# Kernel optimization log

Measured on AMD Instinct MI355X. Metric: run time of the kernel, lower is better.

Reference implementation:

```python
import jax, jax.numpy as jnp
import numpy as np

B, T, S, H = 8, 256, 256, 512


def setup_inputs() -> dict:
    key = jax.random.key(0)
    k1, k2, k3, k4, k5, k6, k7 = jax.random.split(key, 7)
    query = jax.random.normal(k1, (B, T, H), dtype=jnp.float32)
    encoder_outputs = jax.random.normal(k2, (B, S, H), dtype=jnp.float32)
    src_lengths = jax.random.randint(k3, (B,), 1, S + 1)
    src_lengths = src_lengths.at[0].set(S)  # ensure max(lengths) == S (torch code masks to lengths.max())
    scale = 1.0 / np.sqrt(H)
    W_s = jax.random.normal(k4, (H, H), dtype=jnp.float32) * scale      # nn.Linear(H,H) weight
    W_h = jax.random.normal(k5, (H, H), dtype=jnp.float32) * scale
    v = jax.random.normal(k6, (H,), dtype=jnp.float32) * scale          # nn.Linear(H,1) weight
    W_out = jax.random.normal(k7, (H, 2 * H), dtype=jnp.float32) * scale  # nn.Linear(2H,H) weight
    return {"query": query, "encoder_outputs": encoder_outputs, "src_lengths": src_lengths,
            "W_s": W_s, "W_h": W_h, "v": v, "W_out": W_out}


def reference(query, encoder_outputs, src_lengths, W_s, W_h, v, W_out):
    # torch Linear: y = x @ W.T
    Ws_q = jnp.einsum('bth,oh->bto', query, W_s)            # (B,T,H)
    Wh_e = jnp.einsum('bsh,oh->bso', encoder_outputs, W_h)  # (B,S,H)
    # score(i,j) = v^T tanh(Ws_q_j + Wh_e_i), broadcast over (B,T,S,H)
    energies = jnp.einsum('btsh,h->bts',
                          jnp.tanh(Ws_q[:, :, None, :] + Wh_e[:, None, :, :]), v)
    mask = jnp.arange(encoder_outputs.shape[1]) < src_lengths[:, None]  # (B,S)
    energies = jnp.where(mask[:, None, :], energies, -jnp.inf)
    attn_weights = jax.nn.softmax(energies, axis=-1)        # (B,T,S)
    context = jnp.einsum('bts,bsh->bth', attn_weights, encoder_outputs)
    combined = jnp.concatenate([context, query], axis=-1)   # (B,T,2H)
    attn_out = jnp.tanh(jnp.einsum('btk,ok->bto', combined, W_out))
    return attn_out
```

## Files before the change

kernel.cpp:

```cpp
#include <hip/hip_runtime.h>
#include <hip/hip_bf16.h>


typedef __attribute__((ext_vector_type(8))) short bf16x8;
typedef __attribute__((ext_vector_type(4))) float floatx4;

#define C2LOG2E 2.8853900817779268f
#define LOG2E   1.4426950408889634f
#define NEGBIG  -1e30f

__device__ __forceinline__ float fexp2(float x) { return __builtin_amdgcn_exp2f(x); }
__device__ __forceinline__ float frcp(float x)  { return __builtin_amdgcn_rcpf(x); }
__device__ __forceinline__ float ftanh(float x) {
    return 1.0f - 2.0f * frcp(1.0f + fexp2(C2LOG2E * x));
}
__device__ __forceinline__ float fexp2x(float x) {
    return fexp2(C2LOG2E * x);
}

__device__ __forceinline__ unsigned int f2bf_bits(float f) {
    unsigned int u = __float_as_uint(f);
    return (u + 0x7fffu + ((u >> 16) & 1u)) >> 16;
}

typedef const __attribute__((address_space(1))) unsigned int* gas_u32p;
typedef __attribute__((address_space(3))) unsigned int* las_u32p;
__device__ __forceinline__ void gload16(const void* g, void* l) {
    __builtin_amdgcn_global_load_lds((gas_u32p)g, (las_u32p)l, 16, 0, 0);
}

__global__ __launch_bounds__(256) void cast_all_bf16(
    const float* __restrict__ q,  const float* __restrict__ e,
    const float* __restrict__ Ws, const float* __restrict__ Wh,
    const float* __restrict__ Wo,
    unsigned short* __restrict__ qb,  unsigned short* __restrict__ eb,
    unsigned short* __restrict__ Wsb, unsigned short* __restrict__ Whb,
    unsigned short* __restrict__ Wob)
{
    int blk = blockIdx.x;
    const float* src; unsigned short* dst; int base;
    if      (blk < 1024) { src = q;  dst = qb;  base = blk; }
    else if (blk < 2048) { src = e;  dst = eb;  base = blk - 1024; }
    else if (blk < 2304) { src = Ws; dst = Wsb; base = blk - 2048; }
    else if (blk < 2560) { src = Wh; dst = Whb; base = blk - 2304; }
    else                 { src = Wo; dst = Wob; base = blk - 2560; }
    size_t i = (size_t)base * 1024 + threadIdx.x * 4;
    float4 f = *(const float4*)(src + i);
    ushort4 o;
    o.x = (unsigned short)f2bf_bits(f.x);
    o.y = (unsigned short)f2bf_bits(f.y);
    o.z = (unsigned short)f2bf_bits(f.z);
    o.w = (unsigned short)f2bf_bits(f.w);
    *(ushort4*)(dst + i) = o;
}

__global__ __launch_bounds__(256) void gemm32x64_exp_dual(
    const unsigned short* __restrict__ Xa, const unsigned short* __restrict__ Wa,
    float* __restrict__ Ca,
    const unsigned short* __restrict__ Xb, const unsigned short* __restrict__ Wb_,
    float* __restrict__ Cb)
{
    __shared__ unsigned short sA[32 * 64];
    __shared__ unsigned short sB[64 * 64];
    const int K = 512;
    int blk = blockIdx.x;
    const unsigned short* X; const unsigned short* W; float* C;
    int mt, nt, N;
    if (blk < 512) { X = Xa; W = Wa; C = Ca; N = 512;  mt = blk >> 3; nt = blk & 7; }
    else { blk -= 512; X = Xb; W = Wb_; C = Cb; N = 2048; mt = blk >> 5; nt = blk & 31; }
    int row0 = mt * 32, col0 = nt * 64;
    int tid = threadIdx.x, lane = tid & 63, w = tid >> 6;
    int mw = (w & 1) * 16, nw = (w >> 1) * 32;
    int r = lane & 15;

    int lr  = lane >> 3;
    int csw = ((lane & 7) ^ lr) << 3;
    const unsigned short* gA  = X + (size_t)(row0 + 8 * w + lr) * K + csw;
    const unsigned short* gB0 = W + (size_t)(col0 + 16 * w + lr) * K + csw;
    const unsigned short* gB1 = W + (size_t)(col0 + 16 * w + 8 + lr) * K + csw;
    unsigned short* lA  = &sA[w * 512];
    unsigned short* lB0 = &sB[w * 1024];
    unsigned short* lB1 = &sB[w * 1024 + 512];

    int xr = (r & 7) << 4;
    int cq = (lane >> 4) << 4;
    const char* cA = (const char*)sA;
    const char* cB = (const char*)sB;
    int a0 = (mw + r) * 128 + (cq ^ xr);
    int a1 = (mw + r) * 128 + ((cq + 64) ^ xr);
    int b0 = (nw + r) * 128 + (cq ^ xr);
    int b1 = (nw + r) * 128 + ((cq + 64) ^ xr);

    floatx4 acc0 = {0,0,0,0}, acc1 = {0,0,0,0};
    gload16(gA, lA); gload16(gB0, lB0); gload16(gB1, lB1);

    for (int kb = 0; kb < 8; ++kb) {
        __syncthreads();
        bf16x8 af0 = *(const bf16x8*)(cA + a0);
        bf16x8 af1 = *(const bf16x8*)(cA + a1);
        bf16x8 b00 = *(const bf16x8*)(cB + b0);
        bf16x8 b10 = *(const bf16x8*)(cB + b0 + 2048);
        bf16x8 b01 = *(const bf16x8*)(cB + b1);
        bf16x8 b11 = *(const bf16x8*)(cB + b1 + 2048);
        acc0 = __builtin_amdgcn_mfma_f32_16x16x32_bf16(af0, b00, acc0, 0, 0, 0);
        acc1 = __builtin_amdgcn_mfma_f32_16x16x32_bf16(af0, b10, acc1, 0, 0, 0);
        acc0 = __builtin_amdgcn_mfma_f32_16x16x32_bf16(af1, b01, acc0, 0, 0, 0);
        acc1 = __builtin_amdgcn_mfma_f32_16x16x32_bf16(af1, b11, acc1, 0, 0, 0);
        if (kb < 7) {
            __syncthreads();
            gA += 64; gB0 += 64; gB1 += 64;
            gload16(gA, lA); gload16(gB0, lB0); gload16(gB1, lB1);
        }
    }
    int rq = (lane >> 4) * 4;
    float* cp = C + (size_t)(row0 + mw + rq) * N + col0 + nw + r;
#pragma unroll
    for (int i = 0; i < 4; ++i) {
        cp[(size_t)i * N]      = fexp2x(acc0[i]);
        cp[(size_t)i * N + 16] = fexp2x(acc1[i]);
    }
}

#define TQ 4
__global__ __launch_bounds__(512) void energies_v6(
    const float* __restrict__ EA,
    const float* __restrict__ EBT,
    const float* __restrict__ Vv,
    const int* __restrict__ Len,
    float* __restrict__ E)
{
    __shared__ float sA[TQ][516];
    __shared__ float sWn[512];
    __shared__ float sRed[8][TQ][130];

    int tid  = threadIdx.x;
    int lane = tid & 63;
    int w    = tid >> 6;
    int blk  = blockIdx.x;
    int b    = blk >> 7;
    int j    = (blk >> 6) & 1;
    int tq   = blk & 63;
    int len  = Len[b];
    if (j * 128 >= len) return;
    int row0g = b * 256 + tq * TQ;

    {
        int t = tid >> 7, c = (tid & 127) * 4;
        *(float4*)&sA[t][c] = *(const float4*)(EA + (size_t)(row0g + t) * 512 + c);
        sWn[tid] = -2.0f * Vv[tid];
    }
    __syncthreads();

    int h0 = w * 64;
    float acc[TQ][2] = {{0.f}};
    const float* bt = EBT + (size_t)h0 * 2048 + b * 256 + j * 128 + lane;

    float B[8], P[8];
#pragma unroll
    for (int i = 0; i < 4; ++i) {
        B[i]     = bt[(size_t)i * 2048];
        B[i + 4] = bt[(size_t)i * 2048 + 64];
    }
#pragma unroll
    for (int hh = 0; hh < 64; hh += 4) {
        if (hh + 4 < 64) {
            const float* nb = bt + (size_t)(hh + 4) * 2048;
#pragma unroll
            for (int i = 0; i < 4; ++i) {
                P[i]     = nb[(size_t)i * 2048];
                P[i + 4] = nb[(size_t)i * 2048 + 64];
            }
        }
        float4 w4 = *(const float4*)&sWn[h0 + hh];
#pragma unroll
        for (int t = 0; t < TQ; ++t) {
            float4 a4 = *(const float4*)&sA[t][h0 + hh];
#pragma unroll
            for (int u = 0; u < 2; ++u) {
                float d0 = fmaf(a4.x, B[4 * u + 0], 1.0f);
                float d1 = fmaf(a4.y, B[4 * u + 1], 1.0f);
                float d2 = fmaf(a4.z, B[4 * u + 2], 1.0f);
                float d3 = fmaf(a4.w, B[4 * u + 3], 1.0f);
                float num01 = fmaf(w4.x, d1, w4.y * d0);
                float num23 = fmaf(w4.z, d3, w4.w * d2);
                acc[t][u] = fmaf(num01, frcp(d0 * d1), acc[t][u]);
                acc[t][u] = fmaf(num23, frcp(d2 * d3), acc[t][u]);
            }
        }
#pragma unroll
        for (int i = 0; i < 8; ++i) B[i] = P[i];
    }

#pragma unroll
    for (int t = 0; t < TQ; ++t) {
        sRed[w][t][lane]      = acc[t][0];
        sRed[w][t][lane + 64] = acc[t][1];
    }
    __syncthreads();
    {
        int t = tid >> 7, s = tid & 127;
        float sum = 0.f;
#pragma unroll
        for (int ww = 0; ww < 8; ++ww) sum += sRed[ww][t][s];
        E[(size_t)(row0g + t) * 256 + j * 128 + s] = sum;
    }
}

__global__ __launch_bounds__(512) void softmax_ctx_fused(
    const float* __restrict__ E,
    const unsigned short* __restrict__ Eb,
    const int* __restrict__ Len,
    unsigned short* __restrict__ Ctx)
{
    __shared__ unsigned short EncT[64][264];
    __shared__ unsigned short sWb[64][264];
    int tid = threadIdx.x, lane = tid & 63, w = tid >> 6;
    int blk = blockIdx.x;
    int b = blk & 7, hq = (blk >> 3) & 7, tg = blk >> 6;
    int len = Len[b];

    {
        int s = tid >> 1, hg = (tid & 1) * 32;
        const ushort4* src = (const ushort4*)(Eb + (size_t)(b * 256 + s) * 512 + hq * 64 + hg);
#pragma unroll
        for (int k = 0; k < 8; ++k) {
            ushort4 u = src[k];
            EncT[hg + k * 4 + 0][s] = u.x;
            EncT[hg + k * 4 + 1][s] = u.y;
            EncT[hg + k * 4 + 2][s] = u.z;
            EncT[hg + k * 4 + 3][s] = u.w;
        }
    }
    for (int i = 0; i < 8; ++i) {
        int row = w * 8 + i;
        const float* erow = E + (size_t)(b * 256 + tg * 64 + row) * 256;
        float ev[4];
#pragma unroll
        for (int j = 0; j < 4; ++j) {
            int s = lane + 64 * j;
            ev[j] = (s < len) ? erow[s] : NEGBIG;
        }
        float m = fmaxf(fmaxf(ev[0], ev[1]), fmaxf(ev[2], ev[3]));
#pragma unroll
        for (int o = 1; o < 64; o <<= 1) m = fmaxf(m, __shfl_xor(m, o, 64));
        float wv[4], wsum = 0.f;
#pragma unroll
        for (int j = 0; j < 4; ++j) { wv[j] = fexp2((ev[j] - m) * LOG2E); wsum += wv[j]; }
#pragma unroll
        for (int o = 1; o < 64; o <<= 1) wsum += __shfl_xor(wsum, o, 64);
        float inv = frcp(wsum);
#pragma unroll
        for (int j = 0; j < 4; ++j)
            sWb[row][lane + 64 * j] = (unsigned short)f2bf_bits(wv[j] * inv);
    }
    __syncthreads();

    int mt = w & 3, npair = w >> 2;
    int t0 = mt * 16;
    int r  = lane & 15, kq = (lane >> 4) * 8;
    int n0 = npair * 32 + r;
    floatx4 acc0 = {0.f,0.f,0.f,0.f}, acc1 = {0.f,0.f,0.f,0.f};
#pragma unroll
    for (int k = 0; k < 8; ++k) {
        bf16x8 a  = *(const bf16x8*)(&sWb[t0 + r][kq + 32 * k]);
        bf16x8 b0 = *(const bf16x8*)(&EncT[n0][kq + 32 * k]);
        bf16x8 b1 = *(const bf16x8*)(&EncT[n0 + 16][kq + 32 * k]);
        acc0 = __builtin_amdgcn_mfma_f32_16x16x32_bf16(a, b0, acc0, 0, 0, 0);
        acc1 = __builtin_amdgcn_mfma_f32_16x16x32_bf16(a, b1, acc1, 0, 0, 0);
    }
    int row0 = (lane >> 4) * 4;
    unsigned short* op = Ctx + (size_t)(b * 256 + tg * 64 + t0 + row0) * 512 + hq * 64 + npair * 32 + r;
#pragma unroll
    for (int i = 0; i < 4; ++i) {
        op[i * 512]      = (unsigned short)f2bf_bits(acc0[i]);
        op[i * 512 + 16] = (unsigned short)f2bf_bits(acc1[i]);
    }
}

__global__ __launch_bounds__(256) void out_gemm32x64_tanh(
    const unsigned short* __restrict__ Ctx, const unsigned short* __restrict__ Q,
    const unsigned short* __restrict__ Wout, float* __restrict__ Out)
{
    __shared__ unsigned short sA[32 * 64];
    __shared__ unsigned short sB[64 * 64];
    const int N = 512, KW = 1024;
    int blk = blockIdx.x;
    int mt = blk >> 3, nt = blk & 7;
    int row0 = mt * 32, col0 = nt * 64;
    int tid = threadIdx.x, lane = tid & 63, w = tid >> 6;
    int mw = (w & 1) * 16, nw = (w >> 1) * 32;
    int r = lane & 15;

    int lr  = lane >> 3;
    int csw = ((lane & 7) ^ lr) << 3;
    const unsigned short* gactx = Ctx  + (size_t)(row0 + 8 * w + lr) * 512 + csw;
    const unsigned short* gaq   = Q    + (size_t)(row0 + 8 * w + lr) * 512 + csw;
    const unsigned short* gB0   = Wout + (size_t)(col0 + 16 * w + lr) * KW + csw;
    const unsigned short* gB1   = Wout + (size_t)(col0 + 16 * w + 8 + lr) * KW + csw;
    unsigned short* lA  = &sA[w * 512];
    unsigned short* lB0 = &sB[w * 1024];
    unsigned short* lB1 = &sB[w * 1024 + 512];

    int xr = (r & 7) << 4;
    int cq = (lane >> 4) << 4;
    const char* cA = (const char*)sA;
    const char* cB = (const char*)sB;
    int a0 = (mw + r) * 128 + (cq ^ xr);
    int a1 = (mw + r) * 128 + ((cq + 64) ^ xr);
    int b0 = (nw + r) * 128 + (cq ^ xr);
    int b1 = (nw + r) * 128 + ((cq + 64) ^ xr);

    floatx4 acc0 = {0,0,0,0}, acc1 = {0,0,0,0};
    gload16(gactx, lA); gload16(gB0, lB0); gload16(gB1, lB1);

    for (int kb = 0; kb < 16; ++kb) {
        __syncthreads();
        bf16x8 af0 = *(const bf16x8*)(cA + a0);
        bf16x8 af1 = *(const bf16x8*)(cA + a1);
        bf16x8 b00 = *(const bf16x8*)(cB + b0);
        bf16x8 b10 = *(const bf16x8*)(cB + b0 + 2048);
        bf16x8 b01 = *(const bf16x8*)(cB + b1);
        bf16x8 b11 = *(const bf16x8*)(cB + b1 + 2048);
        acc0 = __builtin_amdgcn_mfma_f32_16x16x32_bf16(af0, b00, acc0, 0, 0, 0);
        acc1 = __builtin_amdgcn_mfma_f32_16x16x32_bf16(af0, b10, acc1, 0, 0, 0);
        acc0 = __builtin_amdgcn_mfma_f32_16x16x32_bf16(af1, b01, acc0, 0, 0, 0);
        acc1 = __builtin_amdgcn_mfma_f32_16x16x32_bf16(af1, b11, acc1, 0, 0, 0);
        if (kb < 15) {
            __syncthreads();
            int kn = kb + 1;
            const unsigned short* ga = (kn < 8 ? gactx : gaq) + (kn & 7) * 64;
            gB0 += 64; gB1 += 64;
            gload16(ga, lA); gload16(gB0, lB0); gload16(gB1, lB1);
        }
    }
    int rq = (lane >> 4) * 4;
    float* op = Out + (size_t)(row0 + mw + rq) * N + col0 + nw + r;
#pragma unroll
    for (int i = 0; i < 4; ++i) {
        op[(size_t)i * N]      = ftanh(acc0[i]);
        op[(size_t)i * N + 16] = ftanh(acc1[i]);
    }
}

extern "C" void kernel_launch(void* const* d_in, const int* in_sizes, int n_in,
                              void* d_out, int out_size, void* d_ws, size_t ws_size,
                              hipStream_t stream)
{
    const float* query = (const float*)d_in[0];
    const float* enc   = (const float*)d_in[1];
    const int*   len   = (const int*)d_in[2];
    const float* Ws    = (const float*)d_in[3];
    const float* Wh    = (const float*)d_in[4];
    const float* v     = (const float*)d_in[5];
    const float* Wout  = (const float*)d_in[6];
    float* out = (float*)d_out;

    float* EA   = (float*)d_ws;
    float* EBT  = EA + 2048 * 512;
    float* E    = EBT + 512 * 2048;
    unsigned short* qb  = (unsigned short*)(E + 2048 * 256);
    unsigned short* eb  = qb + 2048 * 512;
    unsigned short* Wsb = eb + 2048 * 512;
    unsigned short* Whb = Wsb + 512 * 512;
    unsigned short* Wob = Whb + 512 * 512;
    unsigned short* ctx = Wob + 512 * 1024;

    cast_all_bf16<<<3072, 256, 0, stream>>>(query, enc, Ws, Wh, Wout,
                                            qb, eb, Wsb, Whb, Wob);
    gemm32x64_exp_dual<<<1024, 256, 0, stream>>>(qb, Wsb, EA, Whb, eb, EBT);
    energies_v6<<<1024, 512, 0, stream>>>(EA, EBT, v, len, E);
    softmax_ctx_fused<<<256, 512, 0, stream>>>(E, eb, len, ctx);
    out_gemm32x64_tanh<<<512, 256, 0, stream>>>(ctx, qb, Wob, out);
}
```

Before: 123.2 us.

## Fuse all five stages into one cooperative persistent kernel with grid syncs

Replaces the five separate kernel launches (cast, dual GEMM, energies, softmax+context, output GEMM) with a single cooperative persistent kernel. Each stage loops over virtual blocks and the stages are separated by grid.sync(). The goal is to remove launch overhead and the gaps between kernels. In exchange it fixes the grid size by occupancy (capped at 512 blocks), uses 66KB of shared memory per block, and pays for four grid-wide barriers. The multi-launch path is kept as a fallback if the cooperative launch fails.

```diff
diff --git a/kernel.cpp b/kernel.cpp
--- a/kernel.cpp
+++ b/kernel.cpp
@@ -1,5 +1,8 @@
 #include <hip/hip_runtime.h>
 #include <hip/hip_bf16.h>
+#include <hip/hip_cooperative_groups.h>
+
+namespace cg = cooperative_groups;
 
 
 typedef __attribute__((ext_vector_type(8))) short bf16x8;
@@ -8,6 +11,7 @@
 #define C2LOG2E 2.8853900817779268f
 #define LOG2E   1.4426950408889634f
 #define NEGBIG  -1e30f
+#define TQ 4
 
 __device__ __forceinline__ float fexp2(float x) { return __builtin_amdgcn_exp2f(x); }
 __device__ __forceinline__ float frcp(float x)  { return __builtin_amdgcn_rcpf(x); }
@@ -27,6 +31,315 @@
 typedef __attribute__((address_space(3))) unsigned int* las_u32p;
 __device__ __forceinline__ void gload16(const void* g, void* l) {
     __builtin_amdgcn_global_load_lds((gas_u32p)g, (las_u32p)l, 16, 0, 0);
+}
+
+__device__ __forceinline__ void cast_range(const float* __restrict__ s,
+                                           unsigned short* __restrict__ d,
+                                           int n4, int gtid, int gs)
+{
+    for (int i = gtid; i < n4; i += gs) {
+        float4 f = ((const float4*)s)[i];
+        ushort4 o;
+        o.x = (unsigned short)f2bf_bits(f.x);
+        o.y = (unsigned short)f2bf_bits(f.y);
+        o.z = (unsigned short)f2bf_bits(f.z);
+        o.w = (unsigned short)f2bf_bits(f.w);
+        ((ushort4*)d)[i] = o;
+    }
+}
+
+__global__ __launch_bounds__(512, 4) void bahdanau_mega(
+    const float* __restrict__ q, const float* __restrict__ e,
+    const int* __restrict__ Len, const float* __restrict__ Ws,
+    const float* __restrict__ Wh, const float* __restrict__ Vv,
+    const float* __restrict__ Wout, float* __restrict__ Out,
+    float* __restrict__ EA, float* __restrict__ EBT, float* __restrict__ E,
+    unsigned short* __restrict__ qb, unsigned short* __restrict__ eb,
+    unsigned short* __restrict__ Wsb, unsigned short* __restrict__ Whb,
+    unsigned short* __restrict__ Wob, unsigned short* __restrict__ ctx)
+{
+    cg::grid_group grid = cg::this_grid();
+    __shared__ __align__(16) char smem[67584];
+
+    const int rb = blockIdx.x, G = gridDim.x;
+    const int tid = threadIdx.x, lane = tid & 63, w = tid >> 6;
+
+    {
+        int gtid = rb * 512 + tid, gs = G * 512;
+        cast_range(q,   qb,  262144, gtid, gs);
+        cast_range(e,   eb,  262144, gtid, gs);
+        cast_range(Ws,  Wsb,  65536, gtid, gs);
+        cast_range(Wh,  Whb,  65536, gtid, gs);
+        cast_range(Wout,Wob, 131072, gtid, gs);
+    }
+    grid.sync();
+
+    {
+        int g = w >> 2, wl = w & 3;
+        unsigned short* sAg = (unsigned short*)(smem + g * 12288);
+        unsigned short* sBg = (unsigned short*)(smem + g * 12288 + 4096);
+        for (int vb = rb * 2 + g; vb < 1024; vb += G * 2) {
+            __syncthreads();
+            int blk = vb;
+            const unsigned short *X, *W; float* C; int mt, nt, N;
+            if (blk < 512) { X = qb; W = Wsb; C = EA; N = 512;  mt = blk >> 3; nt = blk & 7; }
+            else { blk -= 512; X = Whb; W = eb; C = EBT; N = 2048; mt = blk >> 5; nt = blk & 31; }
+            int row0 = mt * 32, col0 = nt * 64;
+            int mw = (wl & 1) * 16, nw = (wl >> 1) * 32;
+            int r = lane & 15;
+            int lr  = lane >> 3;
+            int csw = ((lane & 7) ^ lr) << 3;
+            const unsigned short* gA  = X + (size_t)(row0 + 8 * wl + lr) * 512 + csw;
+            const unsigned short* gB0 = W + (size_t)(col0 + 16 * wl + lr) * 512 + csw;
+            const unsigned short* gB1 = W + (size_t)(col0 + 16 * wl + 8 + lr) * 512 + csw;
+            unsigned short* lA  = sAg + wl * 512;
+            unsigned short* lB0 = sBg + wl * 1024;
+            unsigned short* lB1 = sBg + wl * 1024 + 512;
+            int xr = (r & 7) << 4;
+            int cq = (lane >> 4) << 4;
+            const char* cA = (const char*)sAg;
+            const char* cB = (const char*)sBg;
+            int a0 = (mw + r) * 128 + (cq ^ xr);
+            int a1 = (mw + r) * 128 + ((cq + 64) ^ xr);
+            int b0 = (nw + r) * 128 + (cq ^ xr);
+            int b1 = (nw + r) * 128 + ((cq + 64) ^ xr);
+
+            floatx4 acc0 = {0,0,0,0}, acc1 = {0,0,0,0};
+            gload16(gA, lA); gload16(gB0, lB0); gload16(gB1, lB1);
+
+            for (int kb = 0; kb < 8; ++kb) {
+                __syncthreads();
+                bf16x8 af0 = *(const bf16x8*)(cA + a0);
+                bf16x8 af1 = *(const bf16x8*)(cA + a1);
+                bf16x8 b00 = *(const bf16x8*)(cB + b0);
+                bf16x8 b10 = *(const bf16x8*)(cB + b0 + 2048);
+                bf16x8 b01 = *(const bf16x8*)(cB + b1);
+                bf16x8 b11 = *(const bf16x8*)(cB + b1 + 2048);
+                acc0 = __builtin_amdgcn_mfma_f32_16x16x32_bf16(af0, b00, acc0, 0, 0, 0);
+                acc1 = __builtin_amdgcn_mfma_f32_16x16x32_bf16(af0, b10, acc1, 0, 0, 0);
+                acc0 = __builtin_amdgcn_mfma_f32_16x16x32_bf16(af1, b01, acc0, 0, 0, 0);
+                acc1 = __builtin_amdgcn_mfma_f32_16x16x32_bf16(af1, b11, acc1, 0, 0, 0);
+                if (kb < 7) {
+                    __syncthreads();
+                    gA += 64; gB0 += 64; gB1 += 64;
+                    gload16(gA, lA); gload16(gB0, lB0); gload16(gB1, lB1);
+                }
+            }
+            int rq = (lane >> 4) * 4;
+            float* cp = C + (size_t)(row0 + mw + rq) * N + col0 + nw + r;
+#pragma unroll
+            for (int i = 0; i < 4; ++i) {
+                cp[(size_t)i * N]      = fexp2x(acc0[i]);
+                cp[(size_t)i * N + 16] = fexp2x(acc1[i]);
+            }
+        }
+    }
+    grid.sync();
+
+    {
+        float (*sA)[516] = (float(*)[516])smem;
+        float* sWn = (float*)(smem + 8256);
+        float (*sRed)[TQ][130] = (float(*)[TQ][130])(smem + 10304);
+        for (int vb = rb; vb < 1024; vb += G) {
+            int b  = vb >> 7;
+            int j  = (vb >> 6) & 1;
+            int tq = vb & 63;
+            int len = Len[b];
+            if (j * 128 >= len) continue;
+            int row0g = b * 256 + tq * TQ;
+
+            {
+                int t = tid >> 7, c = (tid & 127) * 4;
+                *(float4*)&sA[t][c] = *(const float4*)(EA + (size_t)(row0g + t) * 512 + c);
+                sWn[tid] = -2.0f * Vv[tid];
+            }
+            __syncthreads();
+
+            int h0 = w * 64;
+            float acc[TQ][2] = {{0.f}};
+            const float* bt = EBT + (size_t)h0 * 2048 + b * 256 + j * 128 + lane;
+
+            float B[8], P[8];
+#pragma unroll
+            for (int i = 0; i < 4; ++i) {
+                B[i]     = bt[(size_t)i * 2048];
+                B[i + 4] = bt[(size_t)i * 2048 + 64];
+            }
+#pragma unroll
+            for (int hh = 0; hh < 64; hh += 4) {
+                if (hh + 4 < 64) {
+                    const float* nb = bt + (size_t)(hh + 4) * 2048;
+#pragma unroll
+                    for (int i = 0; i < 4; ++i) {
+                        P[i]     = nb[(size_t)i * 2048];
+                        P[i + 4] = nb[(size_t)i * 2048 + 64];
+                    }
+                }
+                float4 w4 = *(const float4*)&sWn[h0 + hh];
+#pragma unroll
+                for (int t = 0; t < TQ; ++t) {
+                    float4 a4 = *(const float4*)&sA[t][h0 + hh];
+#pragma unroll
+                    for (int u = 0; u < 2; ++u) {
+                        float d0 = fmaf(a4.x, B[4 * u + 0], 1.0f);
+                        float d1 = fmaf(a4.y, B[4 * u + 1], 1.0f);
+                        float d2 = fmaf(a4.z, B[4 * u + 2], 1.0f);
+                        float d3 = fmaf(a4.w, B[4 * u + 3], 1.0f);
+                        float num01 = fmaf(w4.x, d1, w4.y * d0);
+                        float num23 = fmaf(w4.z, d3, w4.w * d2);
+                        acc[t][u] = fmaf(num01, frcp(d0 * d1), acc[t][u]);
+                        acc[t][u] = fmaf(num23, frcp(d2 * d3), acc[t][u]);
+                    }
+                }
+#pragma unroll
+                for (int i = 0; i < 8; ++i) B[i] = P[i];
+            }
+
+#pragma unroll
+            for (int t = 0; t < TQ; ++t) {
+                sRed[w][t][lane]      = acc[t][0];
+                sRed[w][t][lane + 64] = acc[t][1];
+            }
+            __syncthreads();
+            {
+                int t = tid >> 7, s = tid & 127;
+                float sum = 0.f;
+#pragma unroll
+                for (int ww = 0; ww < 8; ++ww) sum += sRed[ww][t][s];
+                E[(size_t)(row0g + t) * 256 + j * 128 + s] = sum;
+            }
+        }
+    }
+    grid.sync();
+
+    {
+        unsigned short (*EncT)[264] = (unsigned short(*)[264])smem;
+        unsigned short (*sWb)[264]  = (unsigned short(*)[264])(smem + 33792);
+        for (int vb = rb; vb < 256; vb += G) {
+            __syncthreads();
+            int b = vb & 7, hq = (vb >> 3) & 7, tg = vb >> 6;
+            int len = Len[b];
+
+            {
+                int s = tid >> 1, hg = (tid & 1) * 32;
+                const ushort4* src = (const ushort4*)(eb + (size_t)(b * 256 + s) * 512 + hq * 64 + hg);
+#pragma unroll
+                for (int k = 0; k < 8; ++k) {
+                    ushort4 u = src[k];
+                    EncT[hg + k * 4 + 0][s] = u.x;
+                    EncT[hg + k * 4 + 1][s] = u.y;
+                    EncT[hg + k * 4 + 2][s] = u.z;
+                    EncT[hg + k * 4 + 3][s] = u.w;
+                }
+            }
+            for (int i = 0; i < 8; ++i) {
+                int row = w * 8 + i;
+                const float* erow = E + (size_t)(b * 256 + tg * 64 + row) * 256;
+                float ev[4];
+#pragma unroll
+                for (int jj = 0; jj < 4; ++jj) {
+                    int s = lane + 64 * jj;
+                    ev[jj] = (s < len) ? erow[s] : NEGBIG;
+                }
+                float m = fmaxf(fmaxf(ev[0], ev[1]), fmaxf(ev[2], ev[3]));
+#pragma unroll
+                for (int o = 1; o < 64; o <<= 1) m = fmaxf(m, __shfl_xor(m, o, 64));
+                float wv[4], wsum = 0.f;
+#pragma unroll
+                for (int jj = 0; jj < 4; ++jj) { wv[jj] = fexp2((ev[jj] - m) * LOG2E); wsum += wv[jj]; }
+#pragma unroll
+                for (int o = 1; o < 64; o <<= 1) wsum += __shfl_xor(wsum, o, 64);
+                float inv = frcp(wsum);
+#pragma unroll
+                for (int jj = 0; jj < 4; ++jj)
+                    sWb[row][lane + 64 * jj] = (unsigned short)f2bf_bits(wv[jj] * inv);
+            }
+            __syncthreads();
+
+            int mt = w & 3, npair = w >> 2;
+            int t0 = mt * 16;
+            int r  = lane & 15, kq = (lane >> 4) * 8;
+            int n0 = npair * 32 + r;
+            floatx4 acc0 = {0.f,0.f,0.f,0.f}, acc1 = {0.f,0.f,0.f,0.f};
+#pragma unroll
+            for (int k = 0; k < 8; ++k) {
+                bf16x8 a  = *(const bf16x8*)(&sWb[t0 + r][kq + 32 * k]);
+                bf16x8 b0 = *(const bf16x8*)(&EncT[n0][kq + 32 * k]);
+                bf16x8 b1 = *(const bf16x8*)(&EncT[n0 + 16][kq + 32 * k]);
+                acc0 = __builtin_amdgcn_mfma_f32_16x16x32_bf16(a, b0, acc0, 0, 0, 0);
+                acc1 = __builtin_amdgcn_mfma_f32_16x16x32_bf16(a, b1, acc1, 0, 0, 0);
+            }
+            int row0 = (lane >> 4) * 4;
+            unsigned short* op = ctx + (size_t)(b * 256 + tg * 64 + t0 + row0) * 512 + hq * 64 + npair * 32 + r;
+#pragma unroll
+            for (int i = 0; i < 4; ++i) {
+                op[i * 512]      = (unsigned short)f2bf_bits(acc0[i]);
+                op[i * 512 + 16] = (unsigned short)f2bf_bits(acc1[i]);
+            }
+        }
+    }
+    grid.sync();
+
+    {
+        int g = w >> 2, wl = w & 3;
+        unsigned short* sAg = (unsigned short*)(smem + g * 12288);
+        unsigned short* sBg = (unsigned short*)(smem + g * 12288 + 4096);
+        for (int vb = rb * 2 + g; vb < 512; vb += G * 2) {
+            __syncthreads();
+            int mt = vb >> 3, nt = vb & 7;
+            int row0 = mt * 32, col0 = nt * 64;
+            int mw = (wl & 1) * 16, nw = (wl >> 1) * 32;
+            int r = lane & 15;
+            int lr  = lane >> 3;
+            int csw = ((lane & 7) ^ lr) << 3;
+            const unsigned short* gactx = ctx + (size_t)(row0 + 8 * wl + lr) * 512 + csw;
+            const unsigned short* gaq   = qb  + (size_t)(row0 + 8 * wl + lr) * 512 + csw;
+            const unsigned short* gB0   = Wob + (size_t)(col0 + 16 * wl + lr) * 1024 + csw;
+            const unsigned short* gB1   = Wob + (size_t)(col0 + 16 * wl + 8 + lr) * 1024 + csw;
+            unsigned short* lA  = sAg + wl * 512;
+            unsigned short* lB0 = sBg + wl * 1024;
+            unsigned short* lB1 = sBg + wl * 1024 + 512;
+            int xr = (r & 7) << 4;
+            int cq = (lane >> 4) << 4;
+            const char* cA = (const char*)sAg;
+            const char* cB = (const char*)sBg;
+            int a0 = (mw + r) * 128 + (cq ^ xr);
+            int a1 = (mw + r) * 128 + ((cq + 64) ^ xr);
+            int b0 = (nw + r) * 128 + (cq ^ xr);
+            int b1 = (nw + r) * 128 + ((cq + 64) ^ xr);
+
+            floatx4 acc0 = {0,0,0,0}, acc1 = {0,0,0,0};
+            gload16(gactx, lA); gload16(gB0, lB0); gload16(gB1, lB1);
+
+            for (int kb = 0; kb < 16; ++kb) {
+                __syncthreads();
+                bf16x8 af0 = *(const bf16x8*)(cA + a0);
+                bf16x8 af1 = *(const bf16x8*)(cA + a1);
+                bf16x8 b00 = *(const bf16x8*)(cB + b0);
+                bf16x8 b10 = *(const bf16x8*)(cB + b0 + 2048);
+                bf16x8 b01 = *(const bf16x8*)(cB + b1);
+                bf16x8 b11 = *(const bf16x8*)(cB + b1 + 2048);
+                acc0 = __builtin_amdgcn_mfma_f32_16x16x32_bf16(af0, b00, acc0, 0, 0, 0);
+                acc1 = __builtin_amdgcn_mfma_f32_16x16x32_bf16(af0, b10, acc1, 0, 0, 0);
+                acc0 = __builtin_amdgcn_mfma_f32_16x16x32_bf16(af1, b01, acc0, 0, 0, 0);
+                acc1 = __builtin_amdgcn_mfma_f32_16x16x32_bf16(af1, b11, acc1, 0, 0, 0);
+                if (kb < 15) {
+                    __syncthreads();
+                    int kn = kb + 1;
+                    const unsigned short* ga = (kn < 8 ? gactx : gaq) + (kn & 7) * 64;
+                    gB0 += 64; gB1 += 64;
+                    gload16(ga, lA); gload16(gB0, lB0); gload16(gB1, lB1);
+                }
+            }
+            int rq = (lane >> 4) * 4;
+            float* op = Out + (size_t)(row0 + mw + rq) * 512 + col0 + nw + r;
+#pragma unroll
+            for (int i = 0; i < 4; ++i) {
+                op[(size_t)i * 512]      = ftanh(acc0[i]);
+                op[(size_t)i * 512 + 16] = ftanh(acc1[i]);
+            }
+        }
+    }
 }
 
 __global__ __launch_bounds__(256) void cast_all_bf16(
@@ -72,7 +385,6 @@
     int tid = threadIdx.x, lane = tid & 63, w = tid >> 6;
     int mw = (w & 1) * 16, nw = (w >> 1) * 32;
     int r = lane & 15;
-
     int lr  = lane >> 3;
     int csw = ((lane & 7) ^ lr) << 3;
     const unsigned short* gA  = X + (size_t)(row0 + 8 * w + lr) * K + csw;
@@ -81,7 +393,6 @@
     unsigned short* lA  = &sA[w * 512];
     unsigned short* lB0 = &sB[w * 1024];
     unsigned short* lB1 = &sB[w * 1024 + 512];
-
     int xr = (r & 7) << 4;
     int cq = (lane >> 4) << 4;
     const char* cA = (const char*)sA;
@@ -121,12 +432,9 @@
     }
 }
 
-#define TQ 4
 __global__ __launch_bounds__(512) void energies_v6(
-    const float* __restrict__ EA,
-    const float* __restrict__ EBT,
-    const float* __restrict__ Vv,
-    const int* __restrict__ Len,
+    const float* __restrict__ EA, const float* __restrict__ EBT,
+    const float* __restrict__ Vv, const int* __restrict__ Len,
     float* __restrict__ E)
 {
     __shared__ float sA[TQ][516];
@@ -207,10 +515,8 @@
 }
 
 __global__ __launch_bounds__(512) void softmax_ctx_fused(
-    const float* __restrict__ E,
-    const unsigned short* __restrict__ Eb,
-    const int* __restrict__ Len,
-    unsigned short* __restrict__ Ctx)
+    const float* __restrict__ E, const unsigned short* __restrict__ Eb,
+    const int* __restrict__ Len, unsigned short* __restrict__ Ctx)
 {
     __shared__ unsigned short EncT[64][264];
     __shared__ unsigned short sWb[64][264];
@@ -290,7 +596,6 @@
     int tid = threadIdx.x, lane = tid & 63, w = tid >> 6;
     int mw = (w & 1) * 16, nw = (w >> 1) * 32;
     int r = lane & 15;
-
     int lr  = lane >> 3;
     int csw = ((lane & 7) ^ lr) << 3;
     const unsigned short* gactx = Ctx  + (size_t)(row0 + 8 * w + lr) * 512 + csw;
@@ -300,7 +605,6 @@
     unsigned short* lA  = &sA[w * 512];
     unsigned short* lB0 = &sB[w * 1024];
     unsigned short* lB1 = &sB[w * 1024 + 512];
-
     int xr = (r & 7) << 4;
     int cq = (lane >> 4) << 4;
     const char* cA = (const char*)sA;
@@ -365,10 +669,34 @@
     unsigned short* Wob = Whb + 512 * 512;
     unsigned short* ctx = Wob + 512 * 1024;
 
-    cast_all_bf16<<<3072, 256, 0, stream>>>(query, enc, Ws, Wh, Wout,
-                                            qb, eb, Wsb, Whb, Wob);
-    gemm32x64_exp_dual<<<1024, 256, 0, stream>>>(qb, Wsb, EA, Whb, eb, EBT);
-    energies_v6<<<1024, 512, 0, stream>>>(EA, EBT, v, len, E);
-    softmax_ctx_fused<<<256, 512, 0, stream>>>(E, eb, len, ctx);
-    out_gemm32x64_tanh<<<512, 256, 0, stream>>>(ctx, qb, Wob, out);
-}
+    static int coopGrid = -1;
+    if (coopGrid < 0) {
+        int mb = 0;
+        if (hipOccupancyMaxActiveBlocksPerMultiprocessor(&mb, bahdanau_mega, 512, 0)
+                != hipSuccess || mb < 1)
+            mb = 0;
+        coopGrid = mb > 0 ? (mb * 256 > 512 ? 512 : mb * 256) : 0;
+    }
+
+    bool ok = false;
+    if (coopGrid > 0) {
+        void* args[] = { (void*)&query, (void*)&enc, (void*)&len, (void*)&Ws,
+                         (void*)&Wh, (void*)&v, (void*)&Wout, (void*)&out,
+                         (void*)&EA, (void*)&EBT, (void*)&E,
+                         (void*)&qb, (void*)&eb, (void*)&Wsb, (void*)&Whb,
+                         (void*)&Wob, (void*)&ctx };
+        hipError_t rc = hipLaunchCooperativeKernel((const void*)bahdanau_mega,
+                                                   dim3(coopGrid), dim3(512),
+                                                   args, 0, stream);
+        if (rc == hipSuccess) ok = true;
+        else { (void)hipGetLastError(); coopGrid = 0; }
+    }
+    if (!ok) {
+        cast_all_bf16<<<3072, 256, 0, stream>>>(query, enc, Ws, Wh, Wout,
+                                                qb, eb, Wsb, Whb, Wob);
+        gemm32x64_exp_dual<<<1024, 256, 0, stream>>>(qb, Wsb, EA, Whb, eb, EBT);
+        energies_v6<<<1024, 512, 0, stream>>>(EA, EBT, v, len, E);
+        softmax_ctx_fused<<<256, 512, 0, stream>>>(E, eb, len, ctx);
+        out_gemm32x64_tanh<<<512, 256, 0, stream>>>(ctx, qb, Wob, out);
+    }
+}
```

Result: slower. 282.1 us (+128.9%).
